# Optimization experiments

Hardware: AMD Instinct MI355X
Metric: run time of the kernel (lower is better)

Reference implementation:

```python
import jax, jax.numpy as jnp
import numpy as np

N, E, D, C, H1 = 50000, 800000, 128, 8, 2


def setup_inputs() -> dict:
    key = jax.random.key(0)
    ks = jax.random.split(key, 14)
    s = lambda k, sh: (jax.random.normal(k, sh, jnp.float32) * 0.05)
    return {
        "x": jax.random.normal(ks[0], (N, D), jnp.float32),
        "edge_index": jax.random.randint(ks[1], (2, E), 0, N, dtype=jnp.int32),
        # conv1: GATConv(D, D, heads=2, concat=True)
        "W1": s(ks[2], (D, H1 * D)),
        "att1_src": s(ks[3], (H1, D)),
        "att1_dst": s(ks[4], (H1, D)),
        "b1": s(ks[5], (H1 * D,)),
        # conv2: GATConv(2D, D, heads=1, concat=False)
        "W2": s(ks[6], (H1 * D, D)),
        "att2_src": s(ks[7], (1, D)),
        "att2_dst": s(ks[8], (1, D)),
        "b2": s(ks[9], (D,)),
        # MLP head
        "Wm1": s(ks[10], (D, D)),
        "bm1": s(ks[11], (D,)),
        "Wm2": s(ks[12], (D, C)),
        "bm2": s(ks[13], (C,)),
    }


def gat_conv(x, src, dst, W, a_src, a_dst, b, heads, out_ch, concat):
    """PyG GATConv (eval mode): self-loops added by caller, softmax over
    edges grouped by destination node, negative_slope=0.2."""
    n = x.shape[0]
    h = (x @ W).reshape(n, heads, out_ch)              # [N,H,F]
    alpha_src = jnp.einsum('nhf,hf->nh', h, a_src)     # [N,H]
    alpha_dst = jnp.einsum('nhf,hf->nh', h, a_dst)     # [N,H]
    e = jax.nn.leaky_relu(alpha_src[src] + alpha_dst[dst], 0.2)  # [E,H]
    e_max = jax.ops.segment_max(e, dst, num_segments=n)
    ex = jnp.exp(e - e_max[dst])
    denom = jax.ops.segment_sum(ex, dst, num_segments=n)
    alpha = ex / jnp.maximum(denom[dst], 1e-16)        # [E,H]
    out = jax.ops.segment_sum(h[src] * alpha[:, :, None], dst, num_segments=n)
    out = out.reshape(n, heads * out_ch) if concat else out.mean(axis=1)
    return out + b


def reference(x, edge_index, W1, att1_src, att1_dst, b1,
              W2, att2_src, att2_dst, b2, Wm1, bm1, Wm2, bm2):
    n = x.shape[0]
    loop = jnp.arange(n, dtype=edge_index.dtype)
    src = jnp.concatenate([edge_index[0], loop])  # add_self_loops=True
    dst = jnp.concatenate([edge_index[1], loop])
    h = jax.nn.elu(gat_conv(x, src, dst, W1, att1_src, att1_dst, b1, H1, D, True))
    h = jax.nn.elu(gat_conv(h, src, dst, W2, att2_src, att2_dst, b2, 1, D, False))
    h = jax.nn.relu(h @ Wm1 + bm1)
    return jax.nn.relu(h @ Wm2 + bm2)
```

## Files before the change

### kernel.cpp

```cpp
#include <hip/hip_runtime.h>
#include <hip/hip_bf16.h>


__device__ __forceinline__ float lrelu(float x){ return x > 0.f ? x : 0.2f*x; }
__device__ __forceinline__ float elu_f(float x){ return x > 0.f ? x : __expf(x) - 1.f; }
__device__ __forceinline__ unsigned short f2bf(float f){
  __hip_bfloat16 h = __float2bfloat16(f);
  return *reinterpret_cast<unsigned short*>(&h);
}
__device__ __forceinline__ float bflo(unsigned int u){ return __uint_as_float(u << 16); }
__device__ __forceinline__ float bfhi(unsigned int u){ return __uint_as_float(u & 0xffff0000u); }
__device__ __forceinline__ unsigned int packbf(float a, float b){
  return (unsigned int)f2bf(a) | ((unsigned int)f2bf(b) << 16);
}

typedef __attribute__((ext_vector_type(8))) short bf16x8;
typedef __attribute__((ext_vector_type(4))) float f32x4;

__global__ void prep_kernel(const float* __restrict__ W1, unsigned short* __restrict__ BT1a,
                            unsigned short* __restrict__ BT1b,
                            const float* __restrict__ W2, unsigned short* __restrict__ BT2,
                            const float* __restrict__ Wm1, unsigned short* __restrict__ BT3,
                            const float* __restrict__ a1s, const float* __restrict__ a1d,
                            float* __restrict__ va, int* __restrict__ bcount,
                            int* __restrict__ gcur, int NB){
  int idx = blockIdx.x*256 + threadIdx.x;
  const int S1 = 128*256, S2 = 128*256, S3 = 128*128;
  if (idx < S1){
    int k = idx >> 8, c = idx & 255;
    unsigned short v = f2bf(W1[idx]);
    if (c < 128) BT1a[c*128 + k] = v;
    else         BT1b[(c-128)*128 + k] = v;
  } else if (idx < S1 + S2){
    int j = idx - S1;
    int k = j >> 7, n = j & 127;
    BT2[n*256 + k] = f2bf(W2[j]);
  } else if (idx < S1 + S2 + S3){
    int j = idx - S1 - S2;
    int k = j >> 7, n = j & 127;
    BT3[n*128 + k] = f2bf(Wm1[j]);
  } else if (idx < S1 + S2 + S3 + 512){
    int j = idx - S1 - S2 - S3;
    int v = j >> 7, k = j & 127;
    const float* avec = (v < 2) ? a1s : a1d;
    int head = v & 1;
    const float4* wrow = (const float4*)(W1 + (size_t)k*256 + head*128);
    const float4* arow = (const float4*)(avec + head*128);
    float s = 0.f;
    #pragma unroll 8
    for (int f = 0; f < 32; ++f){
      float4 w = wrow[f], a = arow[f];
      s += w.x*a.x + w.y*a.y + w.z*a.z + w.w*a.w;
    }
    va[j] = s;
  } else if (idx < S1 + S2 + S3 + 512 + 2048){
    int z = idx - (S1 + S2 + S3 + 512);
    if (z < 1024){ if (z < NB) bcount[z] = 0; }
    else { z -= 1024; if (z < NB) gcur[z] = 0; }
  }
}

__global__ __launch_bounds__(256) void f2bf_hist_kernel(
    const float* __restrict__ x, unsigned short* __restrict__ xb, int N,
    const float* __restrict__ va, float* __restrict__ as1, float* __restrict__ ad1,
    const int* __restrict__ dst, int E, int* __restrict__ bcount, int NB, int nbConv)
{
  __shared__ int h[1024];
  if ((int)blockIdx.x < nbConv){
    int i = blockIdx.x*256 + threadIdx.x;
    int total = N*32;
    float4 v = make_float4(0.f,0.f,0.f,0.f);
    if (i < total){
      v = ((const float4*)x)[i];
      ushort4 u; u.x=f2bf(v.x); u.y=f2bf(v.y); u.z=f2bf(v.z); u.w=f2bf(v.w);
      ((ushort4*)xb)[i] = u;
    }
    int c = (i & 31) << 2;
    float4 vs0 = *(const float4*)(va + c);
    float4 vs1 = *(const float4*)(va + 128 + c);
    float4 vd0 = *(const float4*)(va + 256 + c);
    float4 vd1 = *(const float4*)(va + 384 + c);
    float s0 = v.x*vs0.x + v.y*vs0.y + v.z*vs0.z + v.w*vs0.w;
    float s1 = v.x*vs1.x + v.y*vs1.y + v.z*vs1.z + v.w*vs1.w;
    float d0 = v.x*vd0.x + v.y*vd0.y + v.z*vd0.z + v.w*vd0.w;
    float d1 = v.x*vd1.x + v.y*vd1.y + v.z*vd1.z + v.w*vd1.w;
    #pragma unroll
    for (int m = 1; m <= 16; m <<= 1){
      s0 += __shfl_xor(s0, m); s1 += __shfl_xor(s1, m);
      d0 += __shfl_xor(d0, m); d1 += __shfl_xor(d1, m);
    }
    if ((i & 31) == 0 && i < total){
      int n = i >> 5;
      *(float2*)(as1 + 2*n) = make_float2(s0, s1);
      *(float2*)(ad1 + 2*n) = make_float2(d0, d1);
    }
  } else {
    for (int i = threadIdx.x; i < NB; i += 256) h[i] = 0;
    __syncthreads();
    int b0 = blockIdx.x - nbConv;
    for (int e = b0*256 + threadIdx.x; e < E; e += 64*256)
      atomicAdd(&h[dst[e] >> 6], 1);
    __syncthreads();
    for (int i = threadIdx.x; i < NB; i += 256)
      if (h[i]) atomicAdd(&bcount[i], h[i]);
  }
}

__global__ __launch_bounds__(256) void bscatter_kernel(
    const int* __restrict__ src, const int* __restrict__ dst, int E,
    const int* __restrict__ bcount, int* __restrict__ boff,
    int* __restrict__ gcur, unsigned int* __restrict__ pairs, int NB)
{
  __shared__ int h[1024];
  __shared__ int runbase[1024];
  __shared__ int sc[1024];
  const int t = threadIdx.x;
  const int e0 = blockIdx.x * 4096;

  for (int i = t; i < 1024; i += 256) sc[i] = (i < NB) ? bcount[i] : 0;
  for (int i = t; i < NB; i += 256) h[i] = 0;
  __syncthreads();
  for (int d = 1; d < 1024; d <<= 1){
    int v0 = (t       >= d) ? sc[t       - d] : 0;
    int v1 = (t + 256 >= d) ? sc[t + 256 - d] : 0;
    int v2 = (t + 512 >= d) ? sc[t + 512 - d] : 0;
    int v3 = (t + 768 >= d) ? sc[t + 768 - d] : 0;
    __syncthreads();
    sc[t] += v0; sc[t+256] += v1; sc[t+512] += v2; sc[t+768] += v3;
    __syncthreads();
  }
  if (blockIdx.x == 0){
    for (int i = t; i <= NB; i += 256) boff[i] = i ? sc[i-1] : 0;
  }

  int myb[16]; unsigned int myw[16];
  #pragma unroll
  for (int q = 0; q < 16; ++q){
    int e = e0 + q*256 + t;
    int b = -1; unsigned int w = 0;
    if (e < E){
      int d = dst[e];
      b = d >> 6;
      w = ((unsigned int)(d & 63) << 26) | (unsigned int)src[e];
      atomicAdd(&h[b], 1);
    }
    myb[q] = b; myw[q] = w;
  }
  __syncthreads();
  for (int i = t; i < NB; i += 256)
    runbase[i] = h[i] ? atomicAdd(&gcur[i], h[i]) : 0;
  __syncthreads();
  for (int i = t; i < NB; i += 256) h[i] = 0;
  __syncthreads();
  #pragma unroll
  for (int q = 0; q < 16; ++q){
    if (myb[q] >= 0){
      int off = atomicAdd(&h[myb[q]], 1);
      int base = myb[q] ? sc[myb[q]-1] : 0;
      pairs[(size_t)base + runbase[myb[q]] + off] = myw[q];
    }
  }
}

__global__ __launch_bounds__(256) void bbuild_kernel(
    const unsigned int* __restrict__ pairs, const int* __restrict__ boff,
    int* __restrict__ rowptr, int* __restrict__ csr, int N)
{
  __shared__ int deg[64], offs[64], cur[64];
  const int b = blockIdx.x;
  const int t = threadIdx.x;
  const int n0 = b << 6;
  const int nNodes = min(64, N - n0);
  const int p0 = boff[b], p1 = boff[b+1];
  const int base = p0 + n0;
  if (t < 64) deg[t] = (t < nNodes) ? 1 : 0;
  __syncthreads();
  for (int i = p0 + t; i < p1; i += 256)
    atomicAdd(&deg[pairs[i] >> 26], 1);
  __syncthreads();
  if (t < 64){
    int x = deg[t];
    #pragma unroll
    for (int d = 1; d < 64; d <<= 1){
      int y = __shfl_up(x, d);
      if (t >= d) x += y;
    }
    offs[t] = x - deg[t];
    cur[t] = 1;
    if (t < nNodes){
      rowptr[n0 + t + 1] = base + x;
      csr[base + x - deg[t]] = n0 + t;
    }
    if (b == 0 && t == 0) rowptr[0] = 0;
  }
  __syncthreads();
  for (int i = p0 + t; i < p1; i += 256){
    unsigned int w = pairs[i];
    int dl = w >> 26;
    int s  = (int)(w & 0x03ffffffu);
    int off = atomicAdd(&cur[dl], 1);
    csr[base + offs[dl] + off] = s;
  }
}

__global__ __launch_bounds__(512, 2) void gemm_conv12_kernel(
    const unsigned short* __restrict__ xa,
    const unsigned short* __restrict__ BT1a, const unsigned short* __restrict__ BT1b,
    const float* __restrict__ b1, const unsigned short* __restrict__ BT2,
    unsigned short* __restrict__ h2b, int M,
    const float* __restrict__ a2s, const float* __restrict__ a2d,
    float* __restrict__ as2, float* __restrict__ ad2)
{
  __shared__ unsigned short t_s[64*264];
  __shared__ unsigned short a_s[64*72];
  __shared__ unsigned short b_s[128*72];
  __shared__ float part_s[64][4];
  __shared__ float part_d[64][4];

  const int tid = threadIdx.x;
  const int lane = tid & 63, wv = tid >> 6;
  const int l15 = lane & 15, quad = lane >> 4;
  const int r0 = blockIdx.x*64;
  const int mh = (wv & 1)*32;
  const int nhp = (wv >> 1)*32;

  const int arow = tid >> 3, askc = tid & 7;
  const int brow = tid >> 2, bc2 = (tid & 3)*2;
  #pragma unroll
  for (int h = 0; h < 2; ++h){
    const unsigned short* BT = h ? BT1b : BT1a;
    f32x4 acc[2][2];
    #pragma unroll
    for (int i = 0; i < 2; ++i)
      #pragma unroll
      for (int j = 0; j < 2; ++j)
        #pragma unroll
        for (int r = 0; r < 4; ++r) acc[i][j][r] = 0.f;

    for (int k0 = 0; k0 < 128; k0 += 64){
      {
        int grow = r0 + arow;
        uint4 v = make_uint4(0u,0u,0u,0u);
        if (grow < M) v = *(const uint4*)(xa + (size_t)grow*256 + h*128 + k0 + askc*8);
        *(uint4*)(&a_s[arow*72 + askc*8]) = v;
      }
      {
        *(uint4*)(&b_s[brow*72 + bc2*8])     = *(const uint4*)(BT + (size_t)brow*128 + k0 + bc2*8);
        *(uint4*)(&b_s[brow*72 + (bc2+1)*8]) = *(const uint4*)(BT + (size_t)brow*128 + k0 + (bc2+1)*8);
      }
      __syncthreads();
      #pragma unroll
      for (int ks = 0; ks < 64; ks += 32){
        bf16x8 af[2], bfr[2];
        #pragma unroll
        for (int i = 0; i < 2; ++i)
          af[i] = *(const bf16x8*)(&a_s[(mh + i*16 + l15)*72 + ks + quad*8]);
        #pragma unroll
        for (int j = 0; j < 2; ++j)
          bfr[j] = *(const bf16x8*)(&b_s[(nhp + j*16 + l15)*72 + ks + quad*8]);
        #pragma unroll
        for (int i = 0; i < 2; ++i)
          #pragma unroll
          for (int j = 0; j < 2; ++j)
            acc[i][j] = __builtin_amdgcn_mfma_f32_16x16x32_bf16(bfr[j], af[i], acc[i][j], 0, 0, 0);
      }
      __syncthreads();
    }
    #pragma unroll
    for (int i = 0; i < 2; ++i){
      int row = mh + i*16 + l15;
      #pragma unroll
      for (int j = 0; j < 2; ++j){
        int n = nhp + j*16 + quad*4;
        float4 bb = *(const float4*)(b1 + h*128 + n);
        ushort4 u;
        u.x = f2bf(elu_f(acc[i][j][0] + bb.x));
        u.y = f2bf(elu_f(acc[i][j][1] + bb.y));
        u.z = f2bf(elu_f(acc[i][j][2] + bb.z));
        u.w = f2bf(elu_f(acc[i][j][3] + bb.w));
        *(ushort4*)(&t_s[row*264 + h*128 + n]) = u;
      }
    }
  }
  __syncthreads();

  f32x4 acc2[2][2];
  #pragma unroll
  for (int i = 0; i < 2; ++i)
    #pragma unroll
    for (int j = 0; j < 2; ++j)
      #pragma unroll
      for (int r = 0; r < 4; ++r) acc2[i][j][r] = 0.f;

  for (int k0 = 0; k0 < 256; k0 += 64){
    {
      *(uint4*)(&b_s[brow*72 + bc2*8])     = *(const uint4*)(BT2 + (size_t)brow*256 + k0 + bc2*8);
      *(uint4*)(&b_s[brow*72 + (bc2+1)*8]) = *(const uint4*)(BT2 + (size_t)brow*256 + k0 + (bc2+1)*8);
    }
    __syncthreads();
    #pragma unroll
    for (int ks = 0; ks < 64; ks += 32){
      bf16x8 af[2], bfr[2];
      #pragma unroll
      for (int i = 0; i < 2; ++i)
        af[i] = *(const bf16x8*)(&t_s[(mh + i*16 + l15)*264 + k0 + ks + quad*8]);
      #pragma unroll
      for (int j = 0; j < 2; ++j)
        bfr[j] = *(const bf16x8*)(&b_s[(nhp + j*16 + l15)*72 + ks + quad*8]);
      #pragma unroll
      for (int i = 0; i < 2; ++i)
        #pragma unroll
        for (int j = 0; j < 2; ++j)
          acc2[i][j] = __builtin_amdgcn_mfma_f32_16x16x32_bf16(bfr[j], af[i], acc2[i][j], 0, 0, 0);
    }
    __syncthreads();
  }

  #pragma unroll
  for (int i = 0; i < 2; ++i){
    int m = r0 + mh + i*16 + l15;
    float ps = 0.f, pd = 0.f;
    #pragma unroll
    for (int j = 0; j < 2; ++j){
      int n = nhp + j*16 + quad*4;
      float4 wsv = *(const float4*)(a2s + n);
      float4 wdv = *(const float4*)(a2d + n);
      float v0 = acc2[i][j][0], v1 = acc2[i][j][1], v2 = acc2[i][j][2], v3 = acc2[i][j][3];
      ps += v0*wsv.x + v1*wsv.y + v2*wsv.z + v3*wsv.w;
      pd += v0*wdv.x + v1*wdv.y + v2*wdv.z + v3*wdv.w;
      if (m < M){
        ushort4 u;
        u.x = f2bf(v0); u.y = f2bf(v1); u.z = f2bf(v2); u.w = f2bf(v3);
        *(ushort4*)(h2b + (size_t)m*128 + n) = u;
      }
    }
    ps += __shfl_xor(ps, 16); ps += __shfl_xor(ps, 32);
    pd += __shfl_xor(pd, 16); pd += __shfl_xor(pd, 32);
    if (quad == 0){
      part_s[mh + i*16 + l15][wv >> 1] = ps;
      part_d[mh + i*16 + l15][wv >> 1] = pd;
    }
  }
  __syncthreads();
  if (tid < 64){
    int gm = r0 + tid;
    if (gm < M){
      as2[gm] = part_s[tid][0] + part_s[tid][1] + part_s[tid][2] + part_s[tid][3];
      ad2[gm] = part_d[tid][0] + part_d[tid][1] + part_d[tid][2] + part_d[tid][3];
    }
  }
}

#define AGG1_FMA(u, a0v, a1v) do{ \
    float f0 = bflo(u.x), f1 = bfhi(u.x), f2v = bflo(u.y), f3 = bfhi(u.y); \
    float f4 = bflo(u.z), f5 = bfhi(u.z), f6 = bflo(u.w), f7 = bfhi(u.w); \
    acc0[0] += a0v*f0; acc0[1] += a0v*f1; acc0[2] += a0v*f2v; acc0[3] += a0v*f3; \
    acc0[4] += a0v*f4; acc0[5] += a0v*f5; acc0[6] += a0v*f6;  acc0[7] += a0v*f7; \
    acc1[0] += a1v*f0; acc1[1] += a1v*f1; acc1[2] += a1v*f2v; acc1[3] += a1v*f3; \
    acc1[4] += a1v*f4; acc1[5] += a1v*f5; acc1[6] += a1v*f6;  acc1[7] += a1v*f7; \
  }while(0)

#define AGG2_FMA(u, av) do{ \
    acc[0] += av*bflo(u.x); acc[1] += av*bfhi(u.x); \
    acc[2] += av*bflo(u.y); acc[3] += av*bfhi(u.y); \
    acc[4] += av*bflo(u.z); acc[5] += av*bfhi(u.z); \
    acc[6] += av*bflo(u.w); acc[7] += av*bfhi(u.w); \
  }while(0)

__global__ __launch_bounds__(256) void agg1x_kernel(
    const unsigned short* __restrict__ xb, const float* __restrict__ as_,
    const float* __restrict__ ad_, const int* __restrict__ rowptr, const int* __restrict__ csr,
    unsigned short* __restrict__ xa, int N)
{
  const int wv = threadIdx.x >> 6, lane = threadIdx.x & 63;
  const int ql = lane & 15;
  const int n = blockIdx.x*16 + wv*4 + (lane >> 4);
  const bool valid = n < N;
  int start = 0, end = 0;
  float2 adv = make_float2(0.f, 0.f);
  if (valid){ start = rowptr[n]; end = rowptr[n+1]; adv = *(const float2*)(ad_ + 2*n); }

  int jl = start + ql;
  bool have = valid && (jl < end);
  int s_l = 0;
  float p0 = 0.f, p1 = 0.f;
  if (have){
    s_l = csr[jl];
    float2 av = *(const float2*)(as_ + 2*s_l);
    p0 = __expf(lrelu(av.x + adv.x));
    p1 = __expf(lrelu(av.y + adv.y));
  }
  float l0 = p0, l1 = p1;
  for (int j = jl + 16; j < end; j += 16){
    int s = csr[j];
    float2 av = *(const float2*)(as_ + 2*s);
    l0 += __expf(lrelu(av.x + adv.x));
    l1 += __expf(lrelu(av.y + adv.y));
  }
  #pragma unroll
  for (int msk = 1; msk <= 8; msk <<= 1){
    l0 += __shfl_xor(l0, msk);
    l1 += __shfl_xor(l1, msk);
  }
  float inv0 = 1.f / fmaxf(l0, 1e-16f);
  float inv1 = 1.f / fmaxf(l1, 1e-16f);
  float a0_l = p0 * inv0;
  float a1_l = p1 * inv1;

  float acc0[8], acc1[8];
  #pragma unroll
  for (int i = 0; i < 8; ++i){ acc0[i] = 0.f; acc1[i] = 0.f; }
  const int c = ql << 3;
  const unsigned short* hp = xb + c;

  #pragma unroll
  for (int half = 0; half < 2; ++half){
    uint4 u[8]; float b0[8], b1[8];
    #pragma unroll
    for (int t = 0; t < 8; ++t){
      int tt = half*8 + t;
      int sA = __shfl(s_l, tt, 16);
      b0[t] = __shfl(a0_l, tt, 16);
      b1[t] = __shfl(a1_l, tt, 16);
      u[t] = *(const uint4*)(hp + (sA << 7));
    }
    #pragma unroll
    for (int t = 0; t < 8; ++t) AGG1_FMA(u[t], b0[t], b1[t]);
  }
  for (int jb = start + 16; jb < end; jb += 16){
    int jl2 = jb + ql;
    int s2 = 0; float a0_2 = 0.f, a1_2 = 0.f;
    if (jl2 < end){
      s2 = csr[jl2];
      float2 av = *(const float2*)(as_ + 2*s2);
      a0_2 = __expf(lrelu(av.x + adv.x)) * inv0;
      a1_2 = __expf(lrelu(av.y + adv.y)) * inv1;
    }
    int cnt2 = min(16, end - jb);
    for (int t2 = 0; t2 < cnt2; t2 += 2){
      int   sA  = __shfl(s2, t2, 16),   sB  = __shfl(s2, t2+1, 16);
      float a0A = __shfl(a0_2, t2, 16), a0B = __shfl(a0_2, t2+1, 16);
      float a1A = __shfl(a1_2, t2, 16), a1B = __shfl(a1_2, t2+1, 16);
      uint4 uA = *(const uint4*)(hp + (sA << 7));
      uint4 uB = *(const uint4*)(hp + (sB << 7));
      AGG1_FMA(uA, a0A, a1A);
      AGG1_FMA(uB, a0B, a1B);
    }
  }

  if (valid){
    uint4 u0, u1;
    u0.x = packbf(acc0[0], acc0[1]); u0.y = packbf(acc0[2], acc0[3]);
    u0.z = packbf(acc0[4], acc0[5]); u0.w = packbf(acc0[6], acc0[7]);
    u1.x = packbf(acc1[0], acc1[1]); u1.y = packbf(acc1[2], acc1[3]);
    u1.z = packbf(acc1[4], acc1[5]); u1.w = packbf(acc1[6], acc1[7]);
    *(uint4*)(xa + (size_t)n*256 + c)       = u0;
    *(uint4*)(xa + (size_t)n*256 + 128 + c) = u1;
  }
}

__global__ __launch_bounds__(256, 4) void agg2mlp_kernel(
    const unsigned short* __restrict__ h2b, const float* __restrict__ as_,
    const float* __restrict__ ad_, const int* __restrict__ rowptr, const int* __restrict__ csr,
    const float* __restrict__ b2, const unsigned short* __restrict__ BT3,
    const float* __restrict__ bm1, const float* __restrict__ Wm2,
    const float* __restrict__ bm2, float* __restrict__ out, int N)
{
  __shared__ unsigned short gb_s[16*136];
  __shared__ float wm2_s[128*8];
  __shared__ float part[16][4][8];
  const int tid = threadIdx.x;
  {
    int i4 = tid*4;
    *(float4*)(&wm2_s[i4]) = *(const float4*)(Wm2 + i4);
  }
  const int wv = tid >> 6, lane = tid & 63;
  const int ql = lane & 15;
  const int g = wv*4 + (lane >> 4);
  const int n = blockIdx.x*16 + g;
  const bool valid = n < N;
  int start = 0, end = 0;
  float adn = 0.f;
  if (valid){ start = rowptr[n]; end = rowptr[n+1]; adn = ad_[n]; }

  int jl = start + ql;
  bool have = valid && (jl < end);
  int s_l = 0;
  float p_l = 0.f;
  if (have){
    s_l = csr[jl];
    p_l = __expf(lrelu(as_[s_l] + adn));
  }
  float l = p_l;
  for (int j = jl + 16; j < end; j += 16)
    l += __expf(lrelu(as_[csr[j]] + adn));
  #pragma unroll
  for (int msk = 1; msk <= 8; msk <<= 1) l += __shfl_xor(l, msk);
  float inv = 1.f / fmaxf(l, 1e-16f);
  float a_l = p_l * inv;

  float acc[8];
  #pragma unroll
  for (int i = 0; i < 8; ++i) acc[i] = 0.f;
  const int c = ql << 3;
  const unsigned short* hp = h2b + c;

  #pragma unroll
  for (int half = 0; half < 2; ++half){
    uint4 u[8]; float av[8];
    #pragma unroll
    for (int t = 0; t < 8; ++t){
      int tt = half*8 + t;
      int sA = __shfl(s_l, tt, 16);
      av[t] = __shfl(a_l, tt, 16);
      u[t] = *(const uint4*)(hp + (sA << 7));
    }
    #pragma unroll
    for (int t = 0; t < 8; ++t) AGG2_FMA(u[t], av[t]);
  }
  for (int jb = start + 16; jb < end; jb += 16){
    int jl2 = jb + ql;
    int s2 = 0; float a2 = 0.f;
    if (jl2 < end){
      s2 = csr[jl2];
      a2 = __expf(lrelu(as_[s2] + adn)) * inv;
    }
    int cnt2 = min(16, end - jb);
    for (int t2 = 0; t2 < cnt2; t2 += 2){
      int   sA = __shfl(s2, t2, 16),  sB = __shfl(s2, t2+1, 16);
      float aA = __shfl(a2, t2, 16),  aB = __shfl(a2, t2+1, 16);
      uint4 uA = *(const uint4*)(hp + (sA << 7));
      uint4 uB = *(const uint4*)(hp + (sB << 7));
      AGG2_FMA(uA, aA);
      AGG2_FMA(uB, aB);
    }
  }

  {
    float4 bb0 = *(const float4*)(b2 + c);
    float4 bb1 = *(const float4*)(b2 + c + 4);
    float o[8];
    o[0]=elu_f(acc[0]+bb0.x); o[1]=elu_f(acc[1]+bb0.y);
    o[2]=elu_f(acc[2]+bb0.z); o[3]=elu_f(acc[3]+bb0.w);
    o[4]=elu_f(acc[4]+bb1.x); o[5]=elu_f(acc[5]+bb1.y);
    o[6]=elu_f(acc[6]+bb1.z); o[7]=elu_f(acc[7]+bb1.w);
    uint4 up;
    up.x = packbf(o[0], o[1]); up.y = packbf(o[2], o[3]);
    up.z = packbf(o[4], o[5]); up.w = packbf(o[6], o[7]);
    *(uint4*)(&gb_s[g*136 + c]) = up;
  }
  __syncthreads();

  const int l15 = lane & 15, quad = lane >> 4;
  const int nh = wv*32;
  f32x4 macc[2];
  #pragma unroll
  for (int j = 0; j < 2; ++j)
    #pragma unroll
    for (int r = 0; r < 4; ++r) macc[j][r] = 0.f;

  #pragma unroll
  for (int ks = 0; ks < 128; ks += 32){
    bf16x8 af = *(const bf16x8*)(&gb_s[l15*136 + ks + quad*8]);
    #pragma unroll
    for (int j = 0; j < 2; ++j){
      bf16x8 bfr = *(const bf16x8*)(BT3 + (size_t)(nh + j*16 + l15)*128 + ks + quad*8);
      macc[j] = __builtin_amdgcn_mfma_f32_16x16x32_bf16(bfr, af, macc[j], 0, 0, 0);
    }
  }

  float po[8];
  #pragma unroll
  for (int o = 0; o < 8; ++o) po[o] = 0.f;
  #pragma unroll
  for (int j = 0; j < 2; ++j){
    int nn = nh + j*16 + quad*4;
    float4 bb = *(const float4*)(bm1 + nn);
    #pragma unroll
    for (int r = 0; r < 4; ++r){
      float hcol = fmaxf(macc[j][r] + ((const float*)&bb)[r], 0.f);
      const float* wr = &wm2_s[(nn + r)*8];
      #pragma unroll
      for (int o = 0; o < 8; ++o) po[o] += hcol*wr[o];
    }
  }
  #pragma unroll
  for (int o = 0; o < 8; ++o){
    po[o] += __shfl_xor(po[o], 16);
    po[o] += __shfl_xor(po[o], 32);
  }
  if (quad == 0){
    #pragma unroll
    for (int o = 0; o < 8; ++o) part[l15][wv][o] = po[o];
  }
  __syncthreads();
  if (tid < 16){
    int gm = blockIdx.x*16 + tid;
    if (gm < N){
      float4 o0, o1;
      o0.x = fmaxf(part[tid][0][0]+part[tid][1][0]+part[tid][2][0]+part[tid][3][0] + bm2[0], 0.f);
      o0.y = fmaxf(part[tid][0][1]+part[tid][1][1]+part[tid][2][1]+part[tid][3][1] + bm2[1], 0.f);
      o0.z = fmaxf(part[tid][0][2]+part[tid][1][2]+part[tid][2][2]+part[tid][3][2] + bm2[2], 0.f);
      o0.w = fmaxf(part[tid][0][3]+part[tid][1][3]+part[tid][2][3]+part[tid][3][3] + bm2[3], 0.f);
      o1.x = fmaxf(part[tid][0][4]+part[tid][1][4]+part[tid][2][4]+part[tid][3][4] + bm2[4], 0.f);
      o1.y = fmaxf(part[tid][0][5]+part[tid][1][5]+part[tid][2][5]+part[tid][3][5] + bm2[5], 0.f);
      o1.z = fmaxf(part[tid][0][6]+part[tid][1][6]+part[tid][2][6]+part[tid][3][6] + bm2[6], 0.f);
      o1.w = fmaxf(part[tid][0][7]+part[tid][1][7]+part[tid][2][7]+part[tid][3][7] + bm2[7], 0.f);
      *(float4*)(out + (size_t)gm*8)     = o0;
      *(float4*)(out + (size_t)gm*8 + 4) = o1;
    }
  }
}

extern "C" void kernel_launch(void* const* d_in, const int* in_sizes, int n_in,
                              void* d_out, int out_size, void* d_ws, size_t ws_size,
                              hipStream_t stream)
{
  (void)n_in; (void)out_size; (void)ws_size;
  const float* x   = (const float*)d_in[0];
  const int*   ei  = (const int*)d_in[1];
  const float* W1  = (const float*)d_in[2];
  const float* a1s = (const float*)d_in[3];
  const float* a1d = (const float*)d_in[4];
  const float* b1  = (const float*)d_in[5];
  const float* W2  = (const float*)d_in[6];
  const float* a2s = (const float*)d_in[7];
  const float* a2d = (const float*)d_in[8];
  const float* b2  = (const float*)d_in[9];
  const float* Wm1 = (const float*)d_in[10];
  const float* bm1 = (const float*)d_in[11];
  const float* Wm2 = (const float*)d_in[12];
  const float* bm2 = (const float*)d_in[13];
  float* out = (float*)d_out;

  const int N = in_sizes[0] / 128;
  const int E = in_sizes[1] / 2;
  const int NB = (N + 63) >> 6;
  const int* srcp = ei;
  const int* dstp = ei + E;

  char* ws = (char*)d_ws;
  unsigned short* xb    = (unsigned short*)ws;
  unsigned short* xa    = (unsigned short*)(ws + (size_t)N*256);
  unsigned short* h2b   = (unsigned short*)(ws + (size_t)N*768);
  char* tail = ws + (size_t)N*1024;
  unsigned short* BT1a = (unsigned short*)tail;
  unsigned short* BT1b = BT1a + 128*128;
  unsigned short* BT2  = BT1b + 128*128;
  unsigned short* BT3  = BT2 + 128*256;
  float* va   = (float*)(BT3 + 128*128);
  float* as1  = va + 512;
  float* ad1  = as1 + (size_t)2*N;
  float* as2  = ad1 + (size_t)2*N;
  float* ad2  = as2 + N;
  int* bcount = (int*)(ad2 + N);
  int* boff   = bcount + 1024;
  int* gcur   = boff + 1032;
  int* rowptr = gcur + 1024;
  int* csr    = rowptr + N + 1;
  unsigned int* pairs = (unsigned int*)(csr + E + N);

  const int nbConv = (N*32 + 255)/256;
  const int prepTotal = 128*256 + 128*256 + 128*128 + 512 + 2048;

  prep_kernel<<<(prepTotal + 255)/256, 256, 0, stream>>>(
      W1, BT1a, BT1b, W2, BT2, Wm1, BT3, a1s, a1d, va, bcount, gcur, NB);
  f2bf_hist_kernel<<<nbConv + 64, 256, 0, stream>>>(x, xb, N, va, as1, ad1,
                                                    dstp, E, bcount, NB, nbConv);
  bscatter_kernel<<<(E + 4095)/4096, 256, 0, stream>>>(srcp, dstp, E, bcount, boff, gcur, pairs, NB);
  bbuild_kernel<<<NB, 256, 0, stream>>>(pairs, boff, rowptr, csr, N);

  const int nb16 = (N + 15) / 16;
  const int g64  = (N + 63) / 64;

  agg1x_kernel<<<nb16, 256, 0, stream>>>(xb, as1, ad1, rowptr, csr, xa, N);
  gemm_conv12_kernel<<<g64, 512, 0, stream>>>(xa, BT1a, BT1b, b1, BT2,
                                              h2b, N, a2s, a2d, as2, ad2);
  agg2mlp_kernel<<<nb16, 256, 0, stream>>>(h2b, as2, ad2, rowptr, csr,
                                           b2, BT3, bm1, Wm2, bm2, out, N);
}
```

Measured before the change: 252.2 us.

## Make MLP head wave-local to drop block-wide syncs in agg2mlp kernel

Each wavefront now runs the full 128-wide MLP matmul on only its own 4 nodes, using a per-wave LDS tile, instead of sharing a 16-node tile across waves split by output columns. This removes the mid-kernel __syncthreads and the cross-wave partial-sum reduction, so waves do not wait on the slowest aggregation in the block. In exchange the MFMA work grows fourfold, since 12 of the 16 rows are padding, each wave loads all of BT3, and the eight accumulators raise register pressure under launch bounds (256,4).

```diff
diff --git a/kernel.cpp b/kernel.cpp
--- a/kernel.cpp
+++ b/kernel.cpp
@@ -466,18 +466,19 @@
     const float* __restrict__ bm1, const float* __restrict__ Wm2,
     const float* __restrict__ bm2, float* __restrict__ out, int N)
 {
-  __shared__ unsigned short gb_s[16*136];
+  __shared__ unsigned short gb_s[4][4*136];
   __shared__ float wm2_s[128*8];
-  __shared__ float part[16][4][8];
   const int tid = threadIdx.x;
   {
     int i4 = tid*4;
     *(float4*)(&wm2_s[i4]) = *(const float4*)(Wm2 + i4);
   }
+  __syncthreads();
+
   const int wv = tid >> 6, lane = tid & 63;
   const int ql = lane & 15;
-  const int g = wv*4 + (lane >> 4);
-  const int n = blockIdx.x*16 + g;
+  const int rw = lane >> 4;
+  const int n = blockIdx.x*16 + wv*4 + rw;
   const bool valid = n < N;
   int start = 0, end = 0;
   float adn = 0.f;
@@ -547,24 +548,24 @@
     uint4 up;
     up.x = packbf(o[0], o[1]); up.y = packbf(o[2], o[3]);
     up.z = packbf(o[4], o[5]); up.w = packbf(o[6], o[7]);
-    *(uint4*)(&gb_s[g*136 + c]) = up;
-  }
-  __syncthreads();
+    *(uint4*)(&gb_s[wv][rw*136 + c]) = up;
+  }
+  asm volatile("" ::: "memory");
 
   const int l15 = lane & 15, quad = lane >> 4;
-  const int nh = wv*32;
-  f32x4 macc[2];
-  #pragma unroll
-  for (int j = 0; j < 2; ++j)
+  const int arow = l15 & 3;
+  f32x4 macc[8];
+  #pragma unroll
+  for (int j = 0; j < 8; ++j)
     #pragma unroll
     for (int r = 0; r < 4; ++r) macc[j][r] = 0.f;
 
   #pragma unroll
   for (int ks = 0; ks < 128; ks += 32){
-    bf16x8 af = *(const bf16x8*)(&gb_s[l15*136 + ks + quad*8]);
-    #pragma unroll
-    for (int j = 0; j < 2; ++j){
-      bf16x8 bfr = *(const bf16x8*)(BT3 + (size_t)(nh + j*16 + l15)*128 + ks + quad*8);
+    bf16x8 af = *(const bf16x8*)(&gb_s[wv][arow*136 + ks + quad*8]);
+    #pragma unroll
+    for (int j = 0; j < 8; ++j){
+      bf16x8 bfr = *(const bf16x8*)(BT3 + (size_t)(j*16 + l15)*128 + ks + quad*8);
       macc[j] = __builtin_amdgcn_mfma_f32_16x16x32_bf16(bfr, af, macc[j], 0, 0, 0);
     }
   }
@@ -573,8 +574,8 @@
   #pragma unroll
   for (int o = 0; o < 8; ++o) po[o] = 0.f;
   #pragma unroll
-  for (int j = 0; j < 2; ++j){
-    int nn = nh + j*16 + quad*4;
+  for (int j = 0; j < 8; ++j){
+    int nn = j*16 + quad*4;
     float4 bb = *(const float4*)(bm1 + nn);
     #pragma unroll
     for (int r = 0; r < 4; ++r){
@@ -589,23 +590,18 @@
     po[o] += __shfl_xor(po[o], 16);
     po[o] += __shfl_xor(po[o], 32);
   }
-  if (quad == 0){
-    #pragma unroll
-    for (int o = 0; o < 8; ++o) part[l15][wv][o] = po[o];
-  }
-  __syncthreads();
-  if (tid < 16){
-    int gm = blockIdx.x*16 + tid;
+  if (quad == 0 && l15 < 4){
+    int gm = blockIdx.x*16 + wv*4 + l15;
     if (gm < N){
       float4 o0, o1;
-      o0.x = fmaxf(part[tid][0][0]+part[tid][1][0]+part[tid][2][0]+part[tid][3][0] + bm2[0], 0.f);
-      o0.y = fmaxf(part[tid][0][1]+part[tid][1][1]+part[tid][2][1]+part[tid][3][1] + bm2[1], 0.f);
-      o0.z = fmaxf(part[tid][0][2]+part[tid][1][2]+part[tid][2][2]+part[tid][3][2] + bm2[2], 0.f);
-      o0.w = fmaxf(part[tid][0][3]+part[tid][1][3]+part[tid][2][3]+part[tid][3][3] + bm2[3], 0.f);
-      o1.x = fmaxf(part[tid][0][4]+part[tid][1][4]+part[tid][2][4]+part[tid][3][4] + bm2[4], 0.f);
-      o1.y = fmaxf(part[tid][0][5]+part[tid][1][5]+part[tid][2][5]+part[tid][3][5] + bm2[5], 0.f);
-      o1.z = fmaxf(part[tid][0][6]+part[tid][1][6]+part[tid][2][6]+part[tid][3][6] + bm2[6], 0.f);
-      o1.w = fmaxf(part[tid][0][7]+part[tid][1][7]+part[tid][2][7]+part[tid][3][7] + bm2[7], 0.f);
+      o0.x = fmaxf(po[0] + bm2[0], 0.f);
+      o0.y = fmaxf(po[1] + bm2[1], 0.f);
+      o0.z = fmaxf(po[2] + bm2[2], 0.f);
+      o0.w = fmaxf(po[3] + bm2[3], 0.f);
+      o1.x = fmaxf(po[4] + bm2[4], 0.f);
+      o1.y = fmaxf(po[5] + bm2[5], 0.f);
+      o1.z = fmaxf(po[6] + bm2[6], 0.f);
+      o1.w = fmaxf(po[7] + bm2[7], 0.f);
       *(float4*)(out + (size_t)gm*8)     = o0;
       *(float4*)(out + (size_t)gm*8 + 4) = o1;
     }
```

Result: slower. 288.0 us (+14.2%).
